# Kernel tuning notes

Hardware: AMD Instinct MI355X
Metric: run time of the kernel (lower is better)

## Reference

```python
import jax, jax.numpy as jnp
import numpy as np
from jax import lax

B, T, I, H = 64, 512, 512, 1024


def setup_inputs() -> dict:
    key = jax.random.key(0)
    k1, k2, k3, k4 = jax.random.split(key, 4)
    # Gates stacked in order: resetgate, updategate, hidden_update (matches forward()).
    inp = jax.random.normal(k1, (B, T, I), dtype=jnp.float32)
    W_in_stacked = jax.random.normal(k2, (I, 3 * H), dtype=jnp.float32) * 0.1
    W_hid_stacked = jax.random.normal(k3, (H, 3 * H), dtype=jnp.float32) * 0.1
    b_stacked = jax.random.normal(k4, (3 * H,), dtype=jnp.float32) * 0.1
    hid_init = jnp.zeros((1, H), dtype=jnp.float32)
    return {"inp": inp, "W_in_stacked": W_in_stacked,
            "W_hid_stacked": W_hid_stacked, "b_stacked": b_stacked,
            "hid_init": hid_init}


def reference(inp, W_in_stacked, W_hid_stacked, b_stacked, hid_init):
    n_units = hid_init.shape[1]
    n_batch = inp.shape[0]
    # Precompute the input contribution for all timesteps (as the original does
    # with one big mm before the loop): [B,T,3H] -> [T,B,3H] seq-first.
    x = jnp.einsum('bti,ig->btg', inp, W_in_stacked) + b_stacked
    x = jnp.swapaxes(x, 0, 1)
    h0 = jnp.broadcast_to(hid_init, (n_batch, n_units))

    def step(h_prev, x_t):
        hid_input = h_prev @ W_hid_stacked  # [B, 3H]
        r = jax.nn.sigmoid(x_t[:, :n_units] + hid_input[:, :n_units])
        u = jax.nn.sigmoid(x_t[:, n_units:2 * n_units]
                           + hid_input[:, n_units:2 * n_units])
        c = jnp.tanh(x_t[:, 2 * n_units:] + r * hid_input[:, 2 * n_units:])
        h_new = (1.0 - u) * h_prev + u * c
        return h_new, None

    h_final, _ = lax.scan(step, h0, x)
    return h_final  # [B, n_units]
```

## Files before the change

### kernel.cpp

```cpp
#include <hip/hip_runtime.h>
#include <hip/hip_fp16.h>
#include <math.h>

typedef _Float16 h16;
typedef __attribute__((ext_vector_type(4))) _Float16 h16x4;
typedef __attribute__((ext_vector_type(8))) _Float16 h16x8;
typedef __attribute__((ext_vector_type(4))) float f32x4;
typedef __attribute__((ext_vector_type(4))) unsigned u32x4;
typedef unsigned long long u64;

#define T_SEQ 512
#define NB    64
#define NI    512
#define NH    1024
#define N3H   3072

#define TAGM 0x0001000100010001ULL

__device__ __forceinline__ u64 cload64(const u64* p) {
  return __hip_atomic_load(p, __ATOMIC_RELAXED, __HIP_MEMORY_SCOPE_AGENT);
}
__device__ __forceinline__ void cstore64(u64* p, u64 v) {
  __hip_atomic_store(p, v, __ATOMIC_RELAXED, __HIP_MEMORY_SCOPE_AGENT);
}
__device__ __forceinline__ u32x4 cload128(const u64* p) {
  u32x4 v;
  asm volatile("global_load_dwordx4 %0, %1, off sc0 sc1" : "=v"(v) : "v"(p));
  return v;
}
#define VMWAIT(N) do { \
  asm volatile("s_waitcnt vmcnt(" #N ")" ::: "memory"); \
  __builtin_amdgcn_sched_barrier(0); \
} while (0)

union H4 { u64 q; h16x4 v; };
union F16B { u32x4 d; u64 q[2]; h16x8 v; };

__device__ __forceinline__ u64 tagpat(unsigned e) {
  return (u64)(e & 1) | ((u64)((e >> 1) & 1) << 16)
       | ((u64)((e >> 2) & 1) << 32) | ((u64)((e >> 3) & 1) << 48);
}


__global__ void gru_init_h(const float* __restrict__ hid0,
                           u64* __restrict__ hfrag) {
  int W = blockIdx.x * blockDim.x + threadIdx.x;
  if (W >= 16384) return;
  int bg = W >> 12;
  int w  = W & 4095;
  int kt = w >> 7;
  int lp = (w >> 1) & 63;
  int q  = w & 1;
  int cb = kt * 32 + (lp >> 4) * 8 + q * 4;
  H4 o;
  #pragma unroll
  for (int j = 0; j < 4; ++j) o.v[j] = (h16)hid0[cb + j];
  hfrag[(size_t)bg * 4096 + w] = o.q & ~TAGM;
}

#define P1_BM 128
#define P1_BK 32

__device__ __forceinline__ int p1swz(int r, int k) {
  return r * P1_BK + ((((k >> 3) ^ (r & 3)) << 3) | (k & 7));
}

__global__ __launch_bounds__(256, 2) void gru_xgemm(
    const float* __restrict__ inp, const float* __restrict__ Win,
    const float* __restrict__ bstk, h16* __restrict__ x) {
  __shared__ h16 sAh[2][P1_BM * P1_BK];
  __shared__ h16 sAl[2][P1_BM * P1_BK];
  __shared__ h16 sBh[2][P1_BM * P1_BK];
  __shared__ h16 sBl[2][P1_BM * P1_BK];

  const int tid = threadIdx.x;
  const int l = tid & 63;
  const int w = tid >> 6;
  const int wm = (w >> 1) * 64, wn = (w & 1) * 64;
  const int mi = blockIdx.x, ni = blockIdx.y;

  const int sr  = tid >> 1;
  const int skh = (tid & 1) * 16;

  const float* aSrcBase = inp + (size_t)(sr & 63) * (T_SEQ * NI)
                              + (size_t)(mi * 2 + (sr >> 6)) * NI + skh;
  const float* bSrcBase = Win + (size_t)skh * N3H + ni * 128 + sr;

  f32x4 acc[4][4] = {};
  float aReg[16];
  float bReg[16];

  auto stage_load = [&](int ks) {
    const float* ap = aSrcBase + ks * P1_BK;
    #pragma unroll
    for (int jg = 0; jg < 4; ++jg) {
      f32x4 v = *(const f32x4*)(ap + jg * 4);
      aReg[jg*4+0] = v[0]; aReg[jg*4+1] = v[1];
      aReg[jg*4+2] = v[2]; aReg[jg*4+3] = v[3];
    }
    const float* bp = bSrcBase + (size_t)ks * P1_BK * N3H;
    #pragma unroll
    for (int j = 0; j < 16; ++j) bReg[j] = bp[(size_t)j * N3H];
  };

  auto stage_write = [&](int buf) {
    #pragma unroll
    for (int jg = 0; jg < 4; ++jg) {
      int idx = p1swz(sr, skh + jg * 4);
      h16x4 hi, lo;
      #pragma unroll
      for (int j = 0; j < 4; ++j) {
        float v = aReg[jg*4+j];
        h16 h = (h16)v; hi[j] = h; lo[j] = (h16)(v - (float)h);
      }
      *(h16x4*)&sAh[buf][idx] = hi;
      *(h16x4*)&sAl[buf][idx] = lo;
      #pragma unroll
      for (int j = 0; j < 4; ++j) {
        float v = bReg[jg*4+j];
        h16 h = (h16)v; hi[j] = h; lo[j] = (h16)(v - (float)h);
      }
      *(h16x4*)&sBh[buf][idx] = hi;
      *(h16x4*)&sBl[buf][idx] = lo;
    }
  };

  auto compute = [&](int buf) {
    const int k0 = (l >> 4) * 8;
    h16x8 bh[4], bl[4];
    #pragma unroll
    for (int nt = 0; nt < 4; ++nt) {
      int idx = p1swz(wn + nt * 16 + (l & 15), k0);
      bh[nt] = *(const h16x8*)&sBh[buf][idx];
      bl[nt] = *(const h16x8*)&sBl[buf][idx];
    }
    #pragma unroll
    for (int mt = 0; mt < 4; ++mt) {
      int idx = p1swz(wm + mt * 16 + (l & 15), k0);
      h16x8 ah = *(const h16x8*)&sAh[buf][idx];
      h16x8 al = *(const h16x8*)&sAl[buf][idx];
      #pragma unroll
      for (int nt = 0; nt < 4; ++nt) {
        acc[mt][nt] = __builtin_amdgcn_mfma_f32_16x16x32_f16(ah, bh[nt], acc[mt][nt], 0, 0, 0);
        acc[mt][nt] = __builtin_amdgcn_mfma_f32_16x16x32_f16(ah, bl[nt], acc[mt][nt], 0, 0, 0);
        acc[mt][nt] = __builtin_amdgcn_mfma_f32_16x16x32_f16(al, bh[nt], acc[mt][nt], 0, 0, 0);
      }
    }
  };

  stage_load(0);
  stage_write(0);
  __syncthreads();
  for (int ks = 0; ks < 16; ++ks) {
    int buf = ks & 1;
    if (ks < 15) stage_load(ks + 1);
    compute(buf);
    if (ks < 15) stage_write(buf ^ 1);
    __syncthreads();
  }

  const int t = mi * 2 + (wm >> 6);
  const int rrb = (l >> 4) * 4;
  #pragma unroll
  for (int nt = 0; nt < 4; ++nt) {
    int colhi = ni * 8 + (wn >> 4) + nt;
    int gg  = colhi >> 6;
    int cgx = colhi & 63;
    float bias = bstk[(colhi << 4) + (l & 15)];
    #pragma unroll
    for (int mt = 0; mt < 4; ++mt) {
      h16x4 v;
      #pragma unroll
      for (int i = 0; i < 4; ++i) v[i] = (h16)(acc[mt][nt][i] + bias);
      size_t idx = ((((size_t)t * 3 + gg) * 64 + cgx) * 4 + mt) * 256
                 + (size_t)(l & 15) * 16 + rrb;
      *(h16x4*)&x[idx] = v;
    }
  }
}

__global__ __launch_bounds__(192, 1) void gru_steps(
    const float* __restrict__ Whid,
    const h16* __restrict__ x,
    u64* __restrict__ hfrag,
    const float* __restrict__ hid0,
    float* __restrict__ out) {
  __shared__ h16 U[3 * 32 * 64 * 8];
  __shared__ h16 tq[16 * 20];

  const int tid = threadIdx.x;
  const int l = tid & 63;
  const int g = tid >> 6;
  const int cg = blockIdx.x & 63;
  const int bg = blockIdx.x >> 6;

  {
    const float* base = Whid + (size_t)g * NH + (size_t)cg * 16 + (l & 15);
    for (int kt = 0; kt < 32; ++kt) {
      const float* src = base + (size_t)(kt * 32 + (l >> 4) * 8) * N3H;
      h16x8 v;
      #pragma unroll
      for (int j = 0; j < 8; ++j) v[j] = (h16)src[(size_t)j * N3H];
      *(h16x8*)&U[(size_t)((g * 32 + kt) * 64 + l) * 8] = v;
    }
  }
  __syncthreads();
  if (g != 0) return;

  const int rr0 = (l >> 4) * 4, cc = l & 15;

  float hq[4];
  {
    float h0 = hid0[cg * 16 + cc];
    #pragma unroll
    for (int i = 0; i < 4; ++i) hq[i] = h0;
  }

  const char* xb0 = (const char*)(x + ((((size_t)0 * 64 + cg) * 4 + bg) * 256)
                                    + (size_t)cc * 16 + rr0);
  const char* xb1 = xb0 + 64 * 4 * 256 * 2;
  const char* xb2 = xb1 + 64 * 4 * 256 * 2;
  u64 xq0 = *(const u64*)xb0, xq1 = *(const u64*)xb1, xq2 = *(const u64*)xb2;

  const int dstw = cg * 64 + ((l >> 4) >> 1) * 32 + (l & 15) * 2 + ((l >> 4) & 1);

  VMWAIT(0);

  for (int s = 1; s <= T_SEQ; ++s) {
    const u64* plane = hfrag + ((size_t)((s - 1) & 1) * 4 + bg) * 4096;
    const u64 patc = tagpat((((unsigned)(s - 1)) >> 1) & 15u);

    f32x4 ac0 = {}, ac1 = {}, ac2 = {};
    F16B W0[8], W1[8], W2[8];

    auto issue = [&](F16B (&W)[8], int c) {
      #pragma unroll
      for (int j = 0; j < 8; ++j)
        W[j].d = cload128(plane + ((size_t)(c * 8 + j) * 64 + l) * 2);
    };
    auto fix = [&](F16B (&W)[8], int c) {
      for (int tries = 0; tries < 30000; ++tries) {
        unsigned bad = 0;
        #pragma unroll
        for (int j = 0; j < 8; ++j)
          bad |= ((((W[j].q[0] ^ patc) | (W[j].q[1] ^ patc)) & TAGM) != 0ULL)
                   ? (1u << j) : 0u;
        if (bad == 0) break;
        if (tries > 4) __builtin_amdgcn_s_sleep(1);
        #pragma unroll
        for (int j = 0; j < 8; ++j)
          if (bad & (1u << j))
            W[j].d = cload128(plane + ((size_t)(c * 8 + j) * 64 + l) * 2);
        VMWAIT(0);
      }
    };
    auto mfmac = [&](F16B (&W)[8], int c) {
      #pragma unroll
      for (int j = 0; j < 8; ++j) {
        int kt = c * 8 + j;
        h16x8 b0 = *(const h16x8*)&U[(size_t)((0 * 32 + kt) * 64 + l) * 8];
        h16x8 b1 = *(const h16x8*)&U[(size_t)((1 * 32 + kt) * 64 + l) * 8];
        h16x8 b2 = *(const h16x8*)&U[(size_t)((2 * 32 + kt) * 64 + l) * 8];
        ac0 = __builtin_amdgcn_mfma_f32_16x16x32_f16(W[j].v, b0, ac0, 0, 0, 0);
        ac1 = __builtin_amdgcn_mfma_f32_16x16x32_f16(W[j].v, b1, ac1, 0, 0, 0);
        ac2 = __builtin_amdgcn_mfma_f32_16x16x32_f16(W[j].v, b2, ac2, 0, 0, 0);
      }
    };

    issue(W0, 0);
    issue(W1, 1);
    VMWAIT(8);
    fix(W0, 0);
    issue(W2, 2);
    mfmac(W0, 0);
    issue(W0, 3);
    VMWAIT(16);
    fix(W1, 1);
    mfmac(W1, 1);
    VMWAIT(8);
    fix(W2, 2);
    mfmac(W2, 2);
    VMWAIT(0);
    fix(W0, 3);
    mfmac(W0, 3);

    H4 xr; xr.q = xq0;
    H4 xu; xu.q = xq1;
    H4 xc; xc.q = xq2;
    #pragma unroll
    for (int i = 0; i < 4; ++i) {
      float r = 1.0f / (1.0f + __expf(-((float)xr.v[i] + ac0[i])));
      float u = 1.0f / (1.0f + __expf(-((float)xu.v[i] + ac1[i])));
      float z = (float)xc.v[i] + r * ac2[i];
      float e = __expf(2.0f * z);
      float c = 1.0f - 2.0f / (e + 1.0f);
      float hn = (1.0f - u) * hq[i] + u * c;
      hq[i] = hn;
      tq[(rr0 + i) * 20 + cc] = (h16)hn;
      if (s == T_SEQ) out[(size_t)(bg * 16 + rr0 + i) * NH + cg * 16 + cc] = hn;
    }

    H4 pv; pv.v = *(const h16x4*)&tq[(l & 15) * 20 + (l >> 4) * 4];
    u64 word = (pv.q & ~TAGM) | tagpat(((unsigned)s >> 1) & 15u);
    u64* outp = hfrag + ((size_t)(s & 1) * 4 + bg) * 4096;
    cstore64(outp + dstw, word);

    if (s < T_SEQ) {
      xq0 = *(const u64*)(xb0 + (size_t)s * 393216);
      xq1 = *(const u64*)(xb1 + (size_t)s * 393216);
      xq2 = *(const u64*)(xb2 + (size_t)s * 393216);
    }
  }
}

extern "C" void kernel_launch(void* const* d_in, const int* in_sizes, int n_in,
                              void* d_out, int out_size, void* d_ws, size_t ws_size,
                              hipStream_t stream) {
  const float* inp  = (const float*)d_in[0];
  const float* Win  = (const float*)d_in[1];
  const float* Whid = (const float*)d_in[2];
  const float* bstk = (const float*)d_in[3];
  const float* hid0 = (const float*)d_in[4];
  float* out = (float*)d_out;

  char* ws = (char*)d_ws;
  const size_t xBytes = (size_t)T_SEQ * NB * N3H * sizeof(h16);
  const size_t hBytes = (size_t)2 * 4 * 4096 * sizeof(u64);
  if (ws_size < xBytes + hBytes) return;

  h16* x = (h16*)ws;
  u64* hfrag = (u64*)(ws + xBytes);

  gru_init_h<<<dim3(16384 / 256), dim3(256), 0, stream>>>(hid0, hfrag);

  dim3 g1(32768 / P1_BM, N3H / 128);
  gru_xgemm<<<g1, dim3(256), 0, stream>>>(inp, Win, bstk, x);

  gru_steps<<<dim3(256), dim3(192), 0, stream>>>(Whid, x, hfrag, hid0, out);
}
```

Baseline: 2.807 ms.

## Pack four column groups per block with register-resident recurrent weights

Work is split differently: each block now runs four waves, one per column group, for a single batch group, so the grid shrinks from 256 to 64 blocks. Each wave holds most of its recurrent weight slice in registers (88 h16x8 vectors), with the remainder kept in LDS. The shared h-state fragment is fetched from global once per block, cooperatively and tag-checked, then staged in double-buffered LDS, rather than every wave loading all of it. The intent is to cut redundant global polling traffic and the LDS weight reads in the step loop. The cost is very high register pressure that may spill, plus an extra block barrier on every step.

```diff
diff --git a/kernel.cpp b/kernel.cpp
--- a/kernel.cpp
+++ b/kernel.cpp
@@ -17,9 +17,6 @@
 
 #define TAGM 0x0001000100010001ULL
 
-__device__ __forceinline__ u64 cload64(const u64* p) {
-  return __hip_atomic_load(p, __ATOMIC_RELAXED, __HIP_MEMORY_SCOPE_AGENT);
-}
 __device__ __forceinline__ void cstore64(u64* p, u64 v) {
   __hip_atomic_store(p, v, __ATOMIC_RELAXED, __HIP_MEMORY_SCOPE_AGENT);
 }
@@ -179,33 +176,60 @@
   }
 }
 
-__global__ __launch_bounds__(192, 1) void gru_steps(
+__global__ __launch_bounds__(256, 1) void gru_steps(
     const float* __restrict__ Whid,
     const h16* __restrict__ x,
     u64* __restrict__ hfrag,
     const float* __restrict__ hid0,
     float* __restrict__ out) {
-  __shared__ h16 U[3 * 32 * 64 * 8];
-  __shared__ h16 tq[16 * 20];
+  __shared__ h16 Albuf[2][16384];
+  __shared__ h16 Bc2[4 * 8 * 64 * 8];
+  __shared__ h16 tq[4][16 * 20];
 
   const int tid = threadIdx.x;
   const int l = tid & 63;
-  const int g = tid >> 6;
-  const int cg = blockIdx.x & 63;
-  const int bg = blockIdx.x >> 6;
-
+  const int w = tid >> 6;
+  const int cg = (blockIdx.x >> 2) * 4 + w;
+  const int bg = blockIdx.x & 3;
+
+  h16x8 Br[32], Bu[32], Bc[24];
   {
-    const float* base = Whid + (size_t)g * NH + (size_t)cg * 16 + (l & 15);
+    const float* b0 = Whid + (size_t)cg * 16 + (l & 15);
+    #pragma unroll
     for (int kt = 0; kt < 32; ++kt) {
-      const float* src = base + (size_t)(kt * 32 + (l >> 4) * 8) * N3H;
+      const float* src = b0 + (size_t)(kt * 32 + (l >> 4) * 8) * N3H;
       h16x8 v;
       #pragma unroll
       for (int j = 0; j < 8; ++j) v[j] = (h16)src[(size_t)j * N3H];
-      *(h16x8*)&U[(size_t)((g * 32 + kt) * 64 + l) * 8] = v;
-    }
-  }
-  __syncthreads();
-  if (g != 0) return;
+      Br[kt] = v;
+    }
+    const float* b1 = b0 + NH;
+    #pragma unroll
+    for (int kt = 0; kt < 32; ++kt) {
+      const float* src = b1 + (size_t)(kt * 32 + (l >> 4) * 8) * N3H;
+      h16x8 v;
+      #pragma unroll
+      for (int j = 0; j < 8; ++j) v[j] = (h16)src[(size_t)j * N3H];
+      Bu[kt] = v;
+    }
+    const float* b2 = b0 + 2 * NH;
+    #pragma unroll
+    for (int kt = 0; kt < 24; ++kt) {
+      const float* src = b2 + (size_t)(kt * 32 + (l >> 4) * 8) * N3H;
+      h16x8 v;
+      #pragma unroll
+      for (int j = 0; j < 8; ++j) v[j] = (h16)src[(size_t)j * N3H];
+      Bc[kt] = v;
+    }
+    #pragma unroll
+    for (int kt = 24; kt < 32; ++kt) {
+      const float* src = b2 + (size_t)(kt * 32 + (l >> 4) * 8) * N3H;
+      h16x8 v;
+      #pragma unroll
+      for (int j = 0; j < 8; ++j) v[j] = (h16)src[(size_t)j * N3H];
+      *(h16x8*)&Bc2[(size_t)((w * 8 + (kt - 24)) * 64 + l) * 8] = v;
+    }
+  }
 
   const int rr0 = (l >> 4) * 4, cc = l & 15;
 
@@ -225,64 +249,72 @@
   const int dstw = cg * 64 + ((l >> 4) >> 1) * 32 + (l & 15) * 2 + ((l >> 4) & 1);
 
   VMWAIT(0);
+  __syncthreads();
 
   for (int s = 1; s <= T_SEQ; ++s) {
-    const u64* plane = hfrag + ((size_t)((s - 1) & 1) * 4 + bg) * 4096;
+    const int par = (s - 1) & 1;
+    const u64* plane = hfrag + ((size_t)par * 4 + bg) * 4096;
     const u64 patc = tagpat((((unsigned)(s - 1)) >> 1) & 15u);
 
+    F16B W0[4], W1[4];
+    #pragma unroll
+    for (int j = 0; j < 4; ++j)
+      W0[j].d = cload128(plane + (size_t)(j * 256 + tid) * 2);
+    #pragma unroll
+    for (int j = 0; j < 4; ++j)
+      W1[j].d = cload128(plane + (size_t)((4 + j) * 256 + tid) * 2);
+
+    VMWAIT(4);
+    for (int tries = 0; tries < 30000; ++tries) {
+      unsigned bad = 0;
+      #pragma unroll
+      for (int j = 0; j < 4; ++j)
+        bad |= ((((W0[j].q[0] ^ patc) | (W0[j].q[1] ^ patc)) & TAGM) != 0ULL)
+                 ? (1u << j) : 0u;
+      if (bad == 0) break;
+      if (tries > 4) __builtin_amdgcn_s_sleep(1);
+      #pragma unroll
+      for (int j = 0; j < 4; ++j)
+        if (bad & (1u << j))
+          W0[j].d = cload128(plane + (size_t)(j * 256 + tid) * 2);
+      VMWAIT(0);
+    }
+    #pragma unroll
+    for (int j = 0; j < 4; ++j)
+      *(h16x8*)&Albuf[par][(size_t)(j * 256 + tid) * 8] = W0[j].v;
+
+    VMWAIT(0);
+    for (int tries = 0; tries < 30000; ++tries) {
+      unsigned bad = 0;
+      #pragma unroll
+      for (int j = 0; j < 4; ++j)
+        bad |= ((((W1[j].q[0] ^ patc) | (W1[j].q[1] ^ patc)) & TAGM) != 0ULL)
+                 ? (1u << j) : 0u;
+      if (bad == 0) break;
+      if (tries > 4) __builtin_amdgcn_s_sleep(1);
+      #pragma unroll
+      for (int j = 0; j < 4; ++j)
+        if (bad & (1u << j))
+          W1[j].d = cload128(plane + (size_t)((4 + j) * 256 + tid) * 2);
+      VMWAIT(0);
+    }
+    #pragma unroll
+    for (int j = 0; j < 4; ++j)
+      *(h16x8*)&Albuf[par][(size_t)((4 + j) * 256 + tid) * 8] = W1[j].v;
+
+    __syncthreads();
+
     f32x4 ac0 = {}, ac1 = {}, ac2 = {};
-    F16B W0[8], W1[8], W2[8];
-
-    auto issue = [&](F16B (&W)[8], int c) {
-      #pragma unroll
-      for (int j = 0; j < 8; ++j)
-        W[j].d = cload128(plane + ((size_t)(c * 8 + j) * 64 + l) * 2);
-    };
-    auto fix = [&](F16B (&W)[8], int c) {
-      for (int tries = 0; tries < 30000; ++tries) {
-        unsigned bad = 0;
-        #pragma unroll
-        for (int j = 0; j < 8; ++j)
-          bad |= ((((W[j].q[0] ^ patc) | (W[j].q[1] ^ patc)) & TAGM) != 0ULL)
-                   ? (1u << j) : 0u;
-        if (bad == 0) break;
-        if (tries > 4) __builtin_amdgcn_s_sleep(1);
-        #pragma unroll
-        for (int j = 0; j < 8; ++j)
-          if (bad & (1u << j))
-            W[j].d = cload128(plane + ((size_t)(c * 8 + j) * 64 + l) * 2);
-        VMWAIT(0);
-      }
-    };
-    auto mfmac = [&](F16B (&W)[8], int c) {
-      #pragma unroll
-      for (int j = 0; j < 8; ++j) {
-        int kt = c * 8 + j;
-        h16x8 b0 = *(const h16x8*)&U[(size_t)((0 * 32 + kt) * 64 + l) * 8];
-        h16x8 b1 = *(const h16x8*)&U[(size_t)((1 * 32 + kt) * 64 + l) * 8];
-        h16x8 b2 = *(const h16x8*)&U[(size_t)((2 * 32 + kt) * 64 + l) * 8];
-        ac0 = __builtin_amdgcn_mfma_f32_16x16x32_f16(W[j].v, b0, ac0, 0, 0, 0);
-        ac1 = __builtin_amdgcn_mfma_f32_16x16x32_f16(W[j].v, b1, ac1, 0, 0, 0);
-        ac2 = __builtin_amdgcn_mfma_f32_16x16x32_f16(W[j].v, b2, ac2, 0, 0, 0);
-      }
-    };
-
-    issue(W0, 0);
-    issue(W1, 1);
-    VMWAIT(8);
-    fix(W0, 0);
-    issue(W2, 2);
-    mfmac(W0, 0);
-    issue(W0, 3);
-    VMWAIT(16);
-    fix(W1, 1);
-    mfmac(W1, 1);
-    VMWAIT(8);
-    fix(W2, 2);
-    mfmac(W2, 2);
-    VMWAIT(0);
-    fix(W0, 3);
-    mfmac(W0, 3);
+    #pragma unroll
+    for (int kt = 0; kt < 32; ++kt) {
+      h16x8 a = *(const h16x8*)&Albuf[par][(size_t)(kt * 64 + l) * 8];
+      ac0 = __builtin_amdgcn_mfma_f32_16x16x32_f16(a, Br[kt], ac0, 0, 0, 0);
+      ac1 = __builtin_amdgcn_mfma_f32_16x16x32_f16(a, Bu[kt], ac1, 0, 0, 0);
+      h16x8 bc = (kt < 24)
+          ? Bc[kt]
+          : *(const h16x8*)&Bc2[(size_t)((w * 8 + (kt - 24)) * 64 + l) * 8];
+      ac2 = __builtin_amdgcn_mfma_f32_16x16x32_f16(a, bc, ac2, 0, 0, 0);
+    }
 
     H4 xr; xr.q = xq0;
     H4 xu; xu.q = xq1;
@@ -296,11 +328,11 @@
       float c = 1.0f - 2.0f / (e + 1.0f);
       float hn = (1.0f - u) * hq[i] + u * c;
       hq[i] = hn;
-      tq[(rr0 + i) * 20 + cc] = (h16)hn;
+      tq[w][(rr0 + i) * 20 + cc] = (h16)hn;
       if (s == T_SEQ) out[(size_t)(bg * 16 + rr0 + i) * NH + cg * 16 + cc] = hn;
     }
 
-    H4 pv; pv.v = *(const h16x4*)&tq[(l & 15) * 20 + (l >> 4) * 4];
+    H4 pv; pv.v = *(const h16x4*)&tq[w][(l & 15) * 20 + (l >> 4) * 4];
     u64 word = (pv.q & ~TAGM) | tagpat(((unsigned)s >> 1) & 15u);
     u64* outp = hfrag + ((size_t)(s & 1) * 4 + bg) * 4096;
     cstore64(outp + dstw, word);
@@ -336,5 +368,5 @@
   dim3 g1(32768 / P1_BM, N3H / 128);
   gru_xgemm<<<g1, dim3(256), 0, stream>>>(inp, Win, bstk, x);
 
-  gru_steps<<<dim3(256), dim3(192), 0, stream>>>(Whid, x, hfrag, hid0, out);
-}
+  gru_steps<<<dim3(64), dim3(256), 0, stream>>>(Whid, x, hfrag, hid0, out);
+}
```

Result: faster. 2.427 ms (-13.5%).
